# Optimization experiments

Measured on AMD Instinct MI355X. Metric: run time of the kernel, lower is better.

Reference implementation:

```python
import jax, jax.numpy as jnp
import numpy as np

B, S, D, HU = 64, 512, 256, 1024
W_SCALE = 0.01  # flax nn.initializers.normal() default stddev


def setup_inputs() -> dict:
    key = jax.random.key(0)
    ks = jax.random.split(key, 13)
    inp = {
        "inputs": jax.random.normal(ks[0], (B, S, D), dtype=jnp.float32),
        "H0": jax.random.normal(ks[1], (B, HU), dtype=jnp.float32),
        "C0": jax.random.normal(ks[2], (B, HU), dtype=jnp.float32),
        "Wxi": jax.random.normal(ks[3], (D, HU), dtype=jnp.float32) * W_SCALE,
        "Whi": jax.random.normal(ks[4], (HU, HU), dtype=jnp.float32) * W_SCALE,
        "bi": jnp.zeros((HU,), dtype=jnp.float32),
        "Wxf": jax.random.normal(ks[5], (D, HU), dtype=jnp.float32) * W_SCALE,
        "Whf": jax.random.normal(ks[6], (HU, HU), dtype=jnp.float32) * W_SCALE,
        "bf": jnp.zeros((HU,), dtype=jnp.float32),
        "Wxo": jax.random.normal(ks[7], (D, HU), dtype=jnp.float32) * W_SCALE,
        "Who": jax.random.normal(ks[8], (HU, HU), dtype=jnp.float32) * W_SCALE,
        "bo": jnp.zeros((HU,), dtype=jnp.float32),
        "Wxc": jax.random.normal(ks[9], (D, HU), dtype=jnp.float32) * W_SCALE,
        "Whc": jax.random.normal(ks[10], (HU, HU), dtype=jnp.float32) * W_SCALE,
        "bc": jnp.zeros((HU,), dtype=jnp.float32),
        "Wd": jax.random.normal(ks[11], (HU, 1), dtype=jnp.float32) * W_SCALE,
        "bd": jnp.zeros((1,), dtype=jnp.float32),
    }
    return inp


def _lstm_forward(inputs, H0, C0, Wxi, Whi, bi, Wxf, Whf, bf,
                  Wxo, Who, bo, Wxc, Whc, bc, Wd, bd):
    Hn = H0.shape[1]
    # Pack the 4 gate projections so the input GEMM is done once for all timesteps.
    Wx = jnp.concatenate([Wxi, Wxf, Wxo, Wxc], axis=1)  # (D, 4H)
    Wh = jnp.concatenate([Whi, Whf, Who, Whc], axis=1)  # (H, 4H)
    b = jnp.concatenate([bi, bf, bo, bc])                # (4H,)
    xg = jnp.einsum('bsd,dk->bsk', inputs, Wx) + b       # (B, S, 4H)

    def step(carry, xg_t):
        H, C = carry
        g = xg_t + H @ Wh                                # (B, 4H)
        i = jax.nn.sigmoid(g[:, :Hn])
        f = jax.nn.sigmoid(g[:, Hn:2 * Hn])
        o = jax.nn.sigmoid(g[:, 2 * Hn:3 * Hn])
        c_tilde = jnp.tanh(g[:, 3 * Hn:])
        C = f * C + i * c_tilde
        H = o * jnp.tanh(C)
        return (H, C), H

    (Hf, Cf), Hs = jax.lax.scan(step, (H0, C0), jnp.swapaxes(xg, 0, 1))
    outputs = jnp.swapaxes(Hs, 0, 1)                     # (B, S, H)
    pred = outputs @ Wd + bd                             # (B, S, 1)
    return pred, (Hf, Cf)


def reference(inputs, H0, C0, Wxi, Whi, bi, Wxf, Whf, bf,
              Wxo, Who, bo, Wxc, Whc, bc, Wd, bd):
    return _lstm_forward(inputs, H0, C0, Wxi, Whi, bi, Wxf, Whf, bf,
                         Wxo, Who, bo, Wxc, Whc, bc, Wd, bd)
```

## Files before the change

### kernel.cpp

```cpp
#include <hip/hip_runtime.h>


#define NB   128
#define SEQ  512
#define BATCH 64
#define DIM  256
#define HU   1024
#define ROWU 1032

typedef unsigned short u16;
typedef unsigned int   u32;
typedef unsigned long long u64;
typedef __attribute__((ext_vector_type(8))) short  short8;
typedef __attribute__((ext_vector_type(4))) float  f32x4;

typedef const __attribute__((address_space(1))) void* gptr_t;
typedef __attribute__((address_space(3))) void*       lptr_t;

__device__ __forceinline__ u16 f2bf(float x) {
  u32 u = __float_as_uint(x);
  u32 r = (u + 0x7FFFu + ((u >> 16) & 1u)) >> 16;
  return (u16)r;
}
__device__ __forceinline__ float sigf(float x)  { return 1.0f / (1.0f + __expf(-x)); }
__device__ __forceinline__ float tanhfast(float x) { return 1.0f - 2.0f / (1.0f + __expf(2.0f * x)); }
__device__ __forceinline__ short8 cv8(uint4 v) {
  union { uint4 d; short8 s; } u; u.d = v; return u.s;
}


__global__ void k_prep(const float* __restrict__ H0, u16* __restrict__ Hbuf0,
                       u32* __restrict__ flags) {
  int i = blockIdx.x * 256 + threadIdx.x;
  if (i < 2048) flags[i] = 0u;
  Hbuf0[i] = f2bf(H0[i]);
}

__global__ void k_xconv(const float* __restrict__ in, u16* __restrict__ out) {
  int i = blockIdx.x * 256 + threadIdx.x;
  float4 v = ((const float4*)in)[i];
  ushort4 o;
  o.x = f2bf(v.x); o.y = f2bf(v.y); o.z = f2bf(v.z); o.w = f2bf(v.w);
  ((ushort4*)out)[i] = o;
}

__global__ void k_pack(const float* __restrict__ Wxi, const float* __restrict__ Whi,
                       const float* __restrict__ Wxf, const float* __restrict__ Whf,
                       const float* __restrict__ Wxo, const float* __restrict__ Who,
                       const float* __restrict__ Wxc, const float* __restrict__ Whc,
                       u16* __restrict__ Wpack) {
  int tid  = blockIdx.x * 256 + threadIdx.x;
  int lane = tid & 63;
  int kc   = (tid >> 6) % 40;
  int nt   = ((tid >> 6) / 40) & 7;
  int bj   = (tid >> 6) / 320;
  int c    = nt * 16 + (lane & 15);
  int gate = (c >> 3) & 3;
  int h    = bj * 32 + (c >> 5) * 8 + (c & 7);
  const float* Wx = (gate == 0) ? Wxi : (gate == 1) ? Wxf : (gate == 2) ? Wxo : Wxc;
  const float* Wh = (gate == 0) ? Whi : (gate == 1) ? Whf : (gate == 2) ? Who : Whc;
  int kbase = kc * 32 + ((lane >> 4) << 3);
  u16 tmp[8];
#pragma unroll
  for (int e = 0; e < 8; e++) {
    int k = kbase + e;
    float v = (k < DIM) ? Wx[k * HU + h] : Wh[(k - DIM) * HU + h];
    tmp[e] = f2bf(v);
  }
  *(uint4*)(Wpack + (size_t)tid * 8) = *(uint4*)tmp;
}

__global__ void k_predsum(const float* __restrict__ part, const float* __restrict__ bd,
                          float* __restrict__ pred) {
  int i = blockIdx.x * 256 + threadIdx.x;
  int b = i & 63, t = i >> 6;
  float s = bd[0];
  const float* p0 = part + (size_t)t * NB * 64 + b;
#pragma unroll 8
  for (int jj = 0; jj < NB; jj++) s += p0[jj * 64];
  pred[b * SEQ + t] = s;
}


struct MainParams {
  const u16* __restrict__ xbf;
  const u16* __restrict__ Wpack;
  u16* __restrict__ Hbuf;
  const float* __restrict__ C0;
  const float* __restrict__ Wd;
  const float* __restrict__ bi;
  const float* __restrict__ bfg;
  const float* __restrict__ bo;
  const float* __restrict__ bc;
  float* __restrict__ ppart;
  float* __restrict__ Hf;
  float* __restrict__ Cf;
  u32* __restrict__ flags;
};

__global__ __launch_bounds__(256, 1) void lstm_main(MainParams p) {
  __shared__ __align__(16) u16 Hsm[16 * ROWU];
  __shared__ __align__(16) u16 Hstg[16 * 32];

  const int tid  = threadIdx.x;
  const int wv   = tid >> 6, lane = tid & 63;
  const int bj   = blockIdx.x >> 2, bb = blockIdx.x & 3;
  const int q    = lane >> 4;
  const int q8   = q * 8;
  const int m16  = lane & 15;
  const int hl   = lane & 7;
  const bool hiH = (lane & 8) != 0;

  const int hglob = bj * 32 + wv * 8 + hl;
  const int row0  = 16 * bb;

  short8 wx[8][2], wh[32][2];
  {
    const u16* wbase = p.Wpack + ((size_t)bj * 8 + 2 * wv) * (40 * 512) + lane * 8;
#pragma unroll
    for (int kc = 0; kc < 8; kc++)
#pragma unroll
      for (int ntl = 0; ntl < 2; ntl++)
        wx[kc][ntl] = *(const short8*)(wbase + ((size_t)ntl * 40 + kc) * 512);
#pragma unroll
    for (int kc = 0; kc < 32; kc++)
#pragma unroll
      for (int ntl = 0; ntl < 2; ntl++)
        wh[kc][ntl] = *(const short8*)(wbase + ((size_t)ntl * 40 + 8 + kc) * 512);
  }

  const float bI = p.bi[hglob],  bF = p.bfg[hglob];
  const float bO = p.bo[hglob],  bC = p.bc[hglob];
  const float wdv = p.Wd[hglob];
  float Cst[4], Hst[4];
#pragma unroll
  for (int r = 0; r < 4; r++) {
    Cst[r] = p.C0[(row0 + q * 4 + r) * HU + hglob];
    Hst[r] = 0.f;
  }

  const u16* Aw = Hsm + m16 * ROWU + q8;

  uint4 ax[8];
#pragma unroll
  for (int kc = 0; kc < 8; kc++)
    ax[kc] = *(const uint4*)(p.xbf + ((size_t)((row0 + m16) * SEQ + 0)) * DIM
                             + kc * 32 + q8);

#pragma unroll 1
  for (int t = 0; t < SEQ; t++) {
    const int rb = t & 1;
    const u16* Hr = p.Hbuf + (size_t)rb * (BATCH * HU);
    u16*       Hw = p.Hbuf + (size_t)(rb ^ 1) * (BATCH * HU);

#pragma unroll
    for (int i = 0; i < 8; i++) {
      int s = wv * 8 + i, row = s >> 1, half = s & 1;
      const u16* g = Hr + (size_t)(row0 + row) * HU + half * 512 + lane * 8;
      __builtin_amdgcn_global_load_lds((gptr_t)(const void*)g,
          (lptr_t)(void*)(Hsm + row * ROWU + half * 512), 16, 0, 17);
    }

    f32x4 acc[2][4];
#pragma unroll
    for (int ntl = 0; ntl < 2; ntl++)
#pragma unroll
      for (int c = 0; c < 4; c++) acc[ntl][c] = (f32x4){0.f, 0.f, 0.f, 0.f};
#pragma unroll
    for (int kc = 0; kc < 8; kc++) {
      short8 af = cv8(ax[kc]);
      acc[0][kc & 3] = __builtin_amdgcn_mfma_f32_16x16x32_bf16(af, wx[kc][0], acc[0][kc & 3], 0, 0, 0);
      acc[1][kc & 3] = __builtin_amdgcn_mfma_f32_16x16x32_bf16(af, wx[kc][1], acc[1][kc & 3], 0, 0, 0);
    }

    __syncthreads();

    {
      const int tn = (t + 1 < SEQ) ? t + 1 : t;
#pragma unroll
      for (int kc = 0; kc < 8; kc++)
        ax[kc] = *(const uint4*)(p.xbf + ((size_t)((row0 + m16) * SEQ + tn)) * DIM
                                 + kc * 32 + q8);
    }

#pragma unroll
    for (int kc = 0; kc < 32; kc++) {
      short8 af = *(const short8*)(Aw + kc * 32);
      acc[0][kc & 3] = __builtin_amdgcn_mfma_f32_16x16x32_bf16(af, wh[kc][0], acc[0][kc & 3], 0, 0, 0);
      acc[1][kc & 3] = __builtin_amdgcn_mfma_f32_16x16x32_bf16(af, wh[kc][1], acc[1][kc & 3], 0, 0, 0);
    }

    f32x4 g01 = (acc[0][0] + acc[0][1]) + (acc[0][2] + acc[0][3]);
    f32x4 g23 = (acc[1][0] + acc[1][1]) + (acc[1][2] + acc[1][3]);

    float pr[4];
#pragma unroll
    for (int r = 0; r < 4; r++) {
      float u0 = g01[r], u1 = g23[r];
      float v0 = __shfl_xor(u0, 8);
      float v1 = __shfl_xor(u1, 8);
      float gi = hiH ? v0 : u0, gf = hiH ? u0 : v0;
      float go = hiH ? v1 : u1, gc = hiH ? u1 : v1;
      float iv = sigf(gi + bI), fv = sigf(gf + bF);
      float ov = sigf(go + bO), ct = tanhfast(gc + bC);
      Cst[r] = fv * Cst[r] + iv * ct;
      Hst[r] = ov * tanhfast(Cst[r]);
      pr[r]  = Hst[r] * wdv;
    }

    if (!hiH) {
#pragma unroll
      for (int r = 0; r < 4; r++)
        Hstg[(q * 4 + r) * 32 + wv * 8 + hl] = f2bf(Hst[r]);
    }

#pragma unroll
    for (int r = 0; r < 4; r++) {
      pr[r] += __shfl_xor(pr[r], 1);
      pr[r] += __shfl_xor(pr[r], 2);
      pr[r] += __shfl_xor(pr[r], 4);
    }
    if (m16 == 0) {
      float4 st = {pr[0], pr[1], pr[2], pr[3]};
      *(float4*)(p.ppart + (((size_t)t * 32 + bj) * 4 + wv) * 64 + row0 + q * 4) = st;
    }

    __syncthreads();

    if (wv == 0) {
#pragma unroll
      for (int g2 = 0; g2 < 2; g2++) {
        int g = g2 * 64 + lane, row = g >> 3, c8 = g & 7;
        u64 v = *(const u64*)&Hstg[row * 32 + c8 * 4];
        __hip_atomic_store((u64*)(Hw + (size_t)(row0 + row) * HU + bj * 32) + c8,
                           v, __ATOMIC_RELAXED, __HIP_MEMORY_SCOPE_AGENT);
      }
      asm volatile("s_waitcnt vmcnt(0)" ::: "memory");
    }

    if (tid == 0)
      __hip_atomic_store(p.flags + (bb * 32 + bj) * 16, (u32)(t + 1),
                         __ATOMIC_RELAXED, __HIP_MEMORY_SCOPE_AGENT);
    if (tid < 32) {
      const u32* f = p.flags + (bb * 32 + tid) * 16;
      while (__hip_atomic_load(f, __ATOMIC_RELAXED, __HIP_MEMORY_SCOPE_AGENT) < (u32)(t + 1))
        __builtin_amdgcn_s_sleep(1);
    }
    __syncthreads();
  }

  if (!hiH) {
#pragma unroll
    for (int r = 0; r < 4; r++) {
      int row = row0 + q * 4 + r;
      p.Hf[row * HU + hglob] = Hst[r];
      p.Cf[row * HU + hglob] = Cst[r];
    }
  }
}


extern "C" void kernel_launch(void* const* d_in, const int* in_sizes, int n_in,
                              void* d_out, int out_size, void* d_ws, size_t ws_size,
                              hipStream_t stream) {
  const float* inputs = (const float*)d_in[0];
  const float* H0  = (const float*)d_in[1];
  const float* C0  = (const float*)d_in[2];
  const float* Wxi = (const float*)d_in[3];
  const float* Whi = (const float*)d_in[4];
  const float* bi  = (const float*)d_in[5];
  const float* Wxf = (const float*)d_in[6];
  const float* Whf = (const float*)d_in[7];
  const float* bf_ = (const float*)d_in[8];
  const float* Wxo = (const float*)d_in[9];
  const float* Who = (const float*)d_in[10];
  const float* bo  = (const float*)d_in[11];
  const float* Wxc = (const float*)d_in[12];
  const float* Whc = (const float*)d_in[13];
  const float* bc  = (const float*)d_in[14];
  const float* Wd  = (const float*)d_in[15];
  const float* bd  = (const float*)d_in[16];

  char* ws = (char*)d_ws;
  u32*   flags = (u32*)ws;
  u16*   Wpack = (u16*)(ws + 8192);
  u16*   xbf   = (u16*)(ws + 8192 + 10485760);
  u16*   Hbuf  = (u16*)(ws + 8192 + 10485760 + 16777216);
  float* ppart = (float*)(ws + 8192 + 10485760 + 16777216 + 262144);

  float* pred = (float*)d_out;
  float* Hf   = pred + BATCH * SEQ;
  float* Cf   = Hf + BATCH * HU;

  k_prep<<<256, 256, 0, stream>>>(H0, Hbuf, flags);
  k_xconv<<<8192, 256, 0, stream>>>(inputs, xbf);
  k_pack<<<2560, 256, 0, stream>>>(Wxi, Whi, Wxf, Whf, Wxo, Who, Wxc, Whc, Wpack);

  MainParams prm{xbf, Wpack, Hbuf, C0, Wd, bi, bf_, bo, bc, ppart, Hf, Cf, flags};
  lstm_main<<<dim3(NB), dim3(256), 0, stream>>>(prm);

  k_predsum<<<128, 256, 0, stream>>>(ppart, bd, pred);
}
```

Measured before the change: 2.501 ms.

## Use per-wave completion flags and spread H stores across all threads

Each wave now publishes its own progress flag instead of one per block. All 256 threads store the bf16 H tile to global memory, replacing the single wave that did it before. The cross-block wait polls 128 per-wave flags, and the second __syncthreads before the spin is replaced by a lighter barrier. The next-step input prefetch is moved after the flag store so it no longer delays signalling. The aim is to shorten the critical path of the per-timestep grid-wide handoff; the cost is four times as many flags, a larger flag area in the workspace, and more polling traffic.

```diff
diff --git a/kernel.cpp b/kernel.cpp
--- a/kernel.cpp
+++ b/kernel.cpp
@@ -27,12 +27,18 @@
 __device__ __forceinline__ short8 cv8(uint4 v) {
   union { uint4 d; short8 s; } u; u.d = v; return u.s;
 }
+__device__ __forceinline__ u32 ld_ag(const u32* p) {
+  return __hip_atomic_load(p, __ATOMIC_RELAXED, __HIP_MEMORY_SCOPE_AGENT);
+}
+__device__ __forceinline__ void st_ag_u32(u32* p, u32 v) {
+  __hip_atomic_store(p, v, __ATOMIC_RELAXED, __HIP_MEMORY_SCOPE_AGENT);
+}
 
 
 __global__ void k_prep(const float* __restrict__ H0, u16* __restrict__ Hbuf0,
                        u32* __restrict__ flags) {
   int i = blockIdx.x * 256 + threadIdx.x;
-  if (i < 2048) flags[i] = 0u;
+  if (i < 8192) flags[i] = 0u;
   Hbuf0[i] = f2bf(H0[i]);
 }
 
@@ -175,14 +181,6 @@
 
     __syncthreads();
 
-    {
-      const int tn = (t + 1 < SEQ) ? t + 1 : t;
-#pragma unroll
-      for (int kc = 0; kc < 8; kc++)
-        ax[kc] = *(const uint4*)(p.xbf + ((size_t)((row0 + m16) * SEQ + tn)) * DIM
-                                 + kc * 32 + q8);
-    }
-
 #pragma unroll
     for (int kc = 0; kc < 32; kc++) {
       short8 af = *(const short8*)(Aw + kc * 32);
@@ -213,6 +211,16 @@
       for (int r = 0; r < 4; r++)
         Hstg[(q * 4 + r) * 32 + wv * 8 + hl] = f2bf(Hst[r]);
     }
+    asm volatile("s_waitcnt lgkmcnt(0)" ::: "memory");
+    __builtin_amdgcn_s_barrier();
+
+    {
+      int row = tid >> 4, cp = tid & 15;
+      u32 v = *(const u32*)&Hstg[row * 32 + cp * 2];
+      __hip_atomic_store((u32*)(Hw + (size_t)(row0 + row) * HU + bj * 32) + cp,
+                         v, __ATOMIC_RELAXED, __HIP_MEMORY_SCOPE_AGENT);
+    }
+    asm volatile("" ::: "memory");
 
 #pragma unroll
     for (int r = 0; r < 4; r++) {
@@ -220,33 +228,30 @@
       pr[r] += __shfl_xor(pr[r], 2);
       pr[r] += __shfl_xor(pr[r], 4);
     }
+
+    asm volatile("s_waitcnt vmcnt(0)" ::: "memory");
+
+    const u32 tf = (u32)(t + 1);
+    if ((tid & 63) == 0)
+      st_ag_u32(p.flags + (((bb * 32 + bj) * 4 + wv) << 4), tf);
+
+    {
+      const int tn = (t + 1 < SEQ) ? t + 1 : t;
+#pragma unroll
+      for (int kc = 0; kc < 8; kc++)
+        ax[kc] = *(const uint4*)(p.xbf + ((size_t)((row0 + m16) * SEQ + tn)) * DIM
+                                 + kc * 32 + q8);
+    }
     if (m16 == 0) {
       float4 st = {pr[0], pr[1], pr[2], pr[3]};
       *(float4*)(p.ppart + (((size_t)t * 32 + bj) * 4 + wv) * 64 + row0 + q * 4) = st;
     }
 
-    __syncthreads();
-
-    if (wv == 0) {
-#pragma unroll
-      for (int g2 = 0; g2 < 2; g2++) {
-        int g = g2 * 64 + lane, row = g >> 3, c8 = g & 7;
-        u64 v = *(const u64*)&Hstg[row * 32 + c8 * 4];
-        __hip_atomic_store((u64*)(Hw + (size_t)(row0 + row) * HU + bj * 32) + c8,
-                           v, __ATOMIC_RELAXED, __HIP_MEMORY_SCOPE_AGENT);
-      }
-      asm volatile("s_waitcnt vmcnt(0)" ::: "memory");
-    }
-
-    if (tid == 0)
-      __hip_atomic_store(p.flags + (bb * 32 + bj) * 16, (u32)(t + 1),
-                         __ATOMIC_RELAXED, __HIP_MEMORY_SCOPE_AGENT);
-    if (tid < 32) {
-      const u32* f = p.flags + (bb * 32 + tid) * 16;
-      while (__hip_atomic_load(f, __ATOMIC_RELAXED, __HIP_MEMORY_SCOPE_AGENT) < (u32)(t + 1))
-        __builtin_amdgcn_s_sleep(1);
-    }
-    __syncthreads();
+    if (tid < 128) {
+      const u32* f = p.flags + (((bb * 32 + (tid & 31)) * 4 + (tid >> 5)) << 4);
+      while (ld_ag(f) < tf) __builtin_amdgcn_s_sleep(1);
+    }
+    __builtin_amdgcn_s_barrier();
   }
 
   if (!hiH) {
@@ -283,10 +288,10 @@
 
   char* ws = (char*)d_ws;
   u32*   flags = (u32*)ws;
-  u16*   Wpack = (u16*)(ws + 8192);
-  u16*   xbf   = (u16*)(ws + 8192 + 10485760);
-  u16*   Hbuf  = (u16*)(ws + 8192 + 10485760 + 16777216);
-  float* ppart = (float*)(ws + 8192 + 10485760 + 16777216 + 262144);
+  u16*   Wpack = (u16*)(ws + 32768);
+  u16*   xbf   = (u16*)(ws + 32768 + 10485760);
+  u16*   Hbuf  = (u16*)(ws + 32768 + 10485760 + 16777216);
+  float* ppart = (float*)(ws + 32768 + 10485760 + 16777216 + 262144);
 
   float* pred = (float*)d_out;
   float* Hf   = pred + BATCH * SEQ;
```

Measured after the change: 2.507 ms. Within noise of the previous version (+0.2%).
